# Kernel optimization log

Measured on AMD Instinct MI355X. Metric: run time of the kernel, lower is better.

## Reference

```python
import jax, jax.numpy as jnp
import numpy as np

B, S, D_MODEL = 2, 2048, 2048
NUM_HEADS, KV_HEADS, HEAD_DIM = 16, 4, 128
KV_DIM = KV_HEADS * HEAD_DIM


def apply_rotary_emb(x, cos, sin):
    # x: [B, S, H, D]; cos/sin: [S, 1, D] broadcast over batch and heads
    xr = x.reshape(*x.shape[:-1], HEAD_DIM // 2, 2)
    x_real, x_imag = xr[..., 0], xr[..., 1]
    x_rot = jnp.stack([-x_imag, x_real], axis=-1).reshape(x.shape)
    return x * cos + x_rot * sin


def setup_inputs() -> dict:
    key = jax.random.key(0)
    k0, k1, k2, k3, k4, k5 = jax.random.split(key, 6)
    hidden_states = jax.random.normal(k0, (B, S, D_MODEL), dtype=jnp.float32)
    attention_mask = jnp.ones((B, S), dtype=bool)
    # realistic rotary angles
    inv_freq = 1.0 / (10000.0 ** (jnp.arange(0, HEAD_DIM, 2, dtype=jnp.float32) / HEAD_DIM))
    angles = jnp.arange(S, dtype=jnp.float32)[:, None] * inv_freq[None, :]  # [S, D/2]
    angles = jnp.repeat(angles, 2, axis=-1)[:, None, :]  # [S, 1, D]
    rope_cos = jnp.cos(angles)
    rope_sin = jnp.sin(angles)
    scale = 0.02
    Wq = jax.random.normal(k1, (D_MODEL, D_MODEL), dtype=jnp.float32) * scale
    Wk = jax.random.normal(k2, (D_MODEL, KV_DIM), dtype=jnp.float32) * scale
    Wv = jax.random.normal(k3, (D_MODEL, KV_DIM), dtype=jnp.float32) * scale
    Wo = jax.random.normal(k4, (D_MODEL, D_MODEL), dtype=jnp.float32) * scale
    return {"hidden_states": hidden_states, "attention_mask": attention_mask,
            "rope_cos": rope_cos, "rope_sin": rope_sin,
            "Wq": Wq, "Wk": Wk, "Wv": Wv, "Wo": Wo}


def reference(hidden_states, attention_mask, rope_cos, rope_sin, Wq, Wk, Wv, Wo):
    b, s, _ = hidden_states.shape
    q = (hidden_states @ Wq).reshape(b, s, NUM_HEADS, HEAD_DIM)
    k = (hidden_states @ Wk).reshape(b, s, KV_HEADS, HEAD_DIM)
    v = (hidden_states @ Wv).reshape(b, s, KV_HEADS, HEAD_DIM)
    # self-attention: RoPE on both Q and K (pre-transpose layout [B,S,H,D])
    q = apply_rotary_emb(q, rope_cos, rope_sin)
    k = apply_rotary_emb(k, rope_cos, rope_sin)
    # GQA: repeat KV heads to match query heads
    n_rep = NUM_HEADS // KV_HEADS
    k = jnp.repeat(k, n_rep, axis=2)  # [B, S, H, D]
    v = jnp.repeat(v, n_rep, axis=2)
    scale = HEAD_DIM ** -0.5
    scores = jnp.einsum("bqhd,bkhd->bhqk", q, k) * scale
    mask = attention_mask[:, None, None, :]  # [B,1,1,S] bool, True = attend
    scores = jnp.where(mask, scores, jnp.finfo(scores.dtype).min)
    probs = jax.nn.softmax(scores, axis=-1)
    out = jnp.einsum("bhqk,bkhd->bqhd", probs, v).reshape(b, s, NUM_HEADS * HEAD_DIM)
    return out @ Wo
```

## Files before the change

kernel.cpp:

```cpp
#include <hip/hip_runtime.h>
#include <hip/hip_fp16.h>

#define DM 2048
#define SL 2048
#define NB 2
#define NH 16
#define NKV 4
#define HD 128
#define QKVN 3072
#define ROWS 4096

using f16 = _Float16;
typedef __attribute__((ext_vector_type(8))) f16 f16x8;
typedef __attribute__((ext_vector_type(4))) f16 f16x4;
typedef __attribute__((ext_vector_type(4))) float f32x4;

__device__ __forceinline__ void gload16(const f16* g, f16* l) {
  __builtin_amdgcn_global_load_lds((const __attribute__((address_space(1))) void*)g,
                                   (__attribute__((address_space(3))) void*)l, 16, 0, 0);
}

__global__ __launch_bounds__(256) void cast_f32_f16(const float* __restrict__ src,
                                                    f16* __restrict__ dst, int n4) {
  int i = blockIdx.x * 256 + threadIdx.x;
  if (i < n4) {
    float4 v = reinterpret_cast<const float4*>(src)[i];
    f16x4 o = {(f16)v.x, (f16)v.y, (f16)v.z, (f16)v.w};
    reinterpret_cast<f16x4*>(dst)[i] = o;
  }
}

__global__ __launch_bounds__(256) void transpose_cast(const float* __restrict__ src,
                                                      f16* __restrict__ dst, int N, float sc) {
  __shared__ float tile[32][33];
  int tx = threadIdx.x & 31, ty = threadIdx.x >> 5;
  int n0 = blockIdx.x * 32, k0 = blockIdx.y * 32;
#pragma unroll
  for (int i = 0; i < 32; i += 8)
    tile[ty + i][tx] = src[(size_t)(k0 + ty + i) * N + n0 + tx];
  __syncthreads();
#pragma unroll
  for (int i = 0; i < 32; i += 8)
    dst[(size_t)(n0 + ty + i) * DM + k0 + tx] = (f16)(tile[tx][ty + i] * sc);
}

__global__ __launch_bounds__(256) void transpose_v(const f16* __restrict__ src,
                                                   f16* __restrict__ dst) {
  __shared__ f16 tl[64 * 64];
  char* tlb = (char*)tl;
  int t = threadIdx.x;
  int r0 = blockIdx.y * 64, c0 = blockIdx.x * 64;
  int lr8 = (t & 7) * 8, hr = t >> 3;
#pragma unroll
  for (int i = 0; i < 64; i += 32) {
    f16x8 v = *(const f16x8*)(src + (size_t)(r0 + hr + i) * QKVN + c0 + lr8);
#pragma unroll
    for (int j = 0; j < 8; ++j) {
      int c = lr8 + j, r = hr + i;
      *(f16*)(tlb + ((c * 128 + r * 2) ^ ((c & 7) << 4))) = v[j];
    }
  }
  __syncthreads();
#pragma unroll
  for (int i = 0; i < 64; i += 32) {
    int c = hr + i;
    f16x8 v = *(const f16x8*)(tlb + ((c * 128 + lr8 * 2) ^ ((c & 7) << 4)));
    *(f16x8*)(dst + (size_t)(c0 + c) * ROWS + r0 + lr8) = v;
  }
}

template <typename TO>
__global__ __launch_bounds__(256) void gemm_kernel(const f16* __restrict__ A,
                                                   const f16* __restrict__ Bt,
                                                   TO* __restrict__ C, int K, int ldc) {
  __shared__ f16 la[128 * 32];
  __shared__ f16 lb[128 * 32];
  int nx = gridDim.x;
  int lin = blockIdx.y * nx + blockIdx.x;
  int cpx = (nx * gridDim.y) >> 3;
  int swz = (lin & 7) * cpx + (lin >> 3);
  int bx = swz % nx, by = swz / nx;
  int t = threadIdx.x;
  int w = t >> 6, lane = t & 63, lr = lane & 15, lg = lane >> 4;
  int wr = (w >> 1) * 64, wc = (w & 1) * 64;
  int rowBase = bx * 128, colBase = by * 128;
  const f16* gA = A + (size_t)(rowBase + (t >> 2)) * K + (t & 3) * 8;
  const f16* gB = Bt + (size_t)(colBase + (t >> 2)) * K + (t & 3) * 8;
  f16* laW = la + w * 512;
  f16* lbW = lb + w * 512;
  f32x4 acc[4][4] = {};
  for (int k0 = 0; k0 < K; k0 += 32) {
    __syncthreads();
    gload16(gA, laW);
    gload16(gA + (size_t)64 * K, laW + 2048);
    gload16(gB, lbW);
    gload16(gB + (size_t)64 * K, lbW + 2048);
    gA += 32; gB += 32;
    __syncthreads();
    f16x8 af[4], bf[4];
#pragma unroll
    for (int m = 0; m < 4; ++m) af[m] = *(const f16x8*)&la[(wr + m * 16 + lr) * 32 + lg * 8];
#pragma unroll
    for (int n = 0; n < 4; ++n) bf[n] = *(const f16x8*)&lb[(wc + n * 16 + lr) * 32 + lg * 8];
#pragma unroll
    for (int m = 0; m < 4; ++m)
#pragma unroll
      for (int n = 0; n < 4; ++n)
        acc[m][n] = __builtin_amdgcn_mfma_f32_16x16x32_f16(af[m], bf[n], acc[m][n], 0, 0, 0);
  }
#pragma unroll
  for (int m = 0; m < 4; ++m) {
    int row = rowBase + wr + m * 16 + lg * 4;
#pragma unroll
    for (int n = 0; n < 4; ++n) {
      int col = colBase + wc + n * 16 + lr;
#pragma unroll
      for (int r = 0; r < 4; ++r)
        C[(size_t)(row + r) * ldc + col] = (TO)acc[m][n][r];
    }
  }
}

__global__ __launch_bounds__(256) void rope_kernel(f16* __restrict__ qk,
                                                   const float* __restrict__ ct,
                                                   const float* __restrict__ st) {
  int idx = blockIdx.x * 256 + threadIdx.x;
  int row = idx / 1280;
  int pc = idx - row * 1280;
  int col = pc * 2;
  int d = col & (HD - 1);
  int s = row & (SL - 1);
  float c = ct[s * HD + d], sn = st[s * HD + d];
  f16* p = qk + (size_t)row * QKVN + col;
  float x0 = (float)p[0], x1 = (float)p[1];
  p[0] = (f16)(x0 * c - x1 * sn);
  p[1] = (f16)(x1 * c + x0 * sn);
}

__global__ __launch_bounds__(256) void attn_kernel(const f16* __restrict__ qk,
                                                   const f16* __restrict__ vt,
                                                   f16* __restrict__ out) {
  __shared__ f16 kl[64 * 128];
  __shared__ f16 vl[128 * 64];
  __shared__ f16 pl[4][16 * 64];
  int bh = blockIdx.y;
  int b = bh >> 4, h = bh & 15, kv = h >> 2;
  int qt = blockIdx.x;
  int t = threadIdx.x, w = t >> 6, lane = t & 63, lr = lane & 15, lg = lane >> 4;

  const f16* Qp = qk + (size_t)(b * SL + qt * 64 + w * 16 + lr) * QKVN + h * HD + lg * 8;
  f16x8 qf[4];
#pragma unroll
  for (int kc = 0; kc < 4; ++kc) qf[kc] = *(const f16x8*)(Qp + kc * 32);

  const f16* Kb = qk + (size_t)(b * SL) * QKVN + DM + kv * HD;
  const f16* Vb = vt + (size_t)(kv * HD) * ROWS + b * SL;

  int kr = t >> 4, kc0 = (t & 15) * 8, kswz = (kr & 7) << 4;
  int vr = t >> 3, vc0 = (t & 7) * 8, vswz = (vr & 7) << 4;
  char* klb = (char*)kl;
  char* vlb = (char*)vl;
  char* kwp = klb + kr * 256 + ((kc0 * 2) ^ kswz);
  char* vwp = vlb + vr * 128 + ((vc0 * 2) ^ vswz);

  f16x8 kreg[4], vreg[4];
#define LOADREGS(KT)                                                              \
  do {                                                                            \
    const f16* kbp = Kb + (size_t)((KT) * 64 + kr) * QKVN + kc0;                  \
    const f16* vbp = Vb + (size_t)vr * ROWS + (KT) * 64 + vc0;                    \
    _Pragma("unroll") for (int it = 0; it < 4; ++it)                              \
        kreg[it] = *(const f16x8*)(kbp + (size_t)it * 16 * QKVN);                 \
    _Pragma("unroll") for (int it = 0; it < 4; ++it)                              \
        vreg[it] = *(const f16x8*)(vbp + (size_t)it * 32 * ROWS);                 \
  } while (0)

  float mrun = -1e30f;
  f32x4 oacc[8] = {};
  f32x4 lacc = {};
  const f16x8 ones = {(f16)1, (f16)1, (f16)1, (f16)1, (f16)1, (f16)1, (f16)1, (f16)1};

  char* plb = (char*)pl[w];
  int swzr = (lr & 7) << 4;

  LOADREGS(0);
  for (int kt = 0; kt < SL / 64; ++kt) {
    __syncthreads();
#pragma unroll
    for (int it = 0; it < 4; ++it) *(f16x8*)(kwp + it * 4096) = kreg[it];
#pragma unroll
    for (int it = 0; it < 4; ++it) *(f16x8*)(vwp + it * 4096) = vreg[it];
    __syncthreads();
    if (kt < SL / 64 - 1) LOADREGS(kt + 1);
    f32x4 s[4] = {};
    __builtin_amdgcn_s_setprio(1);
#pragma unroll
    for (int kc = 0; kc < 4; ++kc) {
#pragma unroll
      for (int ct = 0; ct < 4; ++ct) {
        f16x8 kf = *(const f16x8*)(klb + (ct * 16 + lr) * 256 + ((kc * 64 + lg * 16) ^ swzr));
        s[ct] = __builtin_amdgcn_mfma_f32_16x16x32_f16(kf, qf[kc], s[ct], 0, 0, 0);
      }
    }
    __builtin_amdgcn_s_setprio(0);
    float vmax = -1e30f;
#pragma unroll
    for (int ct = 0; ct < 4; ++ct)
      vmax = fmaxf(vmax, fmaxf(fmaxf(s[ct][0], s[ct][1]), fmaxf(s[ct][2], s[ct][3])));
    vmax = fmaxf(vmax, __shfl_xor(vmax, 16, 64));
    vmax = fmaxf(vmax, __shfl_xor(vmax, 32, 64));
    if (!__all(vmax <= mrun + 6.f)) {
      float mnew = fmaxf(mrun, vmax);
      float al = exp2f(mrun - mnew);
#pragma unroll
      for (int dtl = 0; dtl < 8; ++dtl)
#pragma unroll
        for (int r = 0; r < 4; ++r) oacc[dtl][r] *= al;
#pragma unroll
      for (int r = 0; r < 4; ++r) lacc[r] *= al;
      mrun = mnew;
    }
    float m = mrun;
#pragma unroll
    for (int ct = 0; ct < 4; ++ct) {
      f16x4 pv = {(f16)exp2f(s[ct][0] - m), (f16)exp2f(s[ct][1] - m),
                  (f16)exp2f(s[ct][2] - m), (f16)exp2f(s[ct][3] - m)};
      *(f16x4*)(plb + lr * 128 + ((ct * 32 + lg * 8) ^ swzr)) = pv;
    }
    __builtin_amdgcn_s_setprio(1);
#pragma unroll
    for (int kc = 0; kc < 2; ++kc) {
      f16x8 pf = *(const f16x8*)(plb + lr * 128 + ((kc * 64 + lg * 16) ^ swzr));
      lacc = __builtin_amdgcn_mfma_f32_16x16x32_f16(ones, pf, lacc, 0, 0, 0);
#pragma unroll
      for (int dtl = 0; dtl < 8; ++dtl) {
        f16x8 vf = *(const f16x8*)(vlb + (dtl * 16 + lr) * 128 + ((kc * 64 + lg * 16) ^ swzr));
        oacc[dtl] = __builtin_amdgcn_mfma_f32_16x16x32_f16(vf, pf, oacc[dtl], 0, 0, 0);
      }
    }
    __builtin_amdgcn_s_setprio(0);
  }
#undef LOADREGS
  float inv = 1.0f / lacc[0];
  f16* orow = out + (size_t)(b * SL + qt * 64 + w * 16 + lr) * DM + h * HD;
#pragma unroll
  for (int dtl = 0; dtl < 8; ++dtl) {
    f16x4 o = {(f16)(oacc[dtl][0] * inv), (f16)(oacc[dtl][1] * inv),
               (f16)(oacc[dtl][2] * inv), (f16)(oacc[dtl][3] * inv)};
    *(f16x4*)(orow + dtl * 16 + lg * 4) = o;
  }
}

extern "C" void kernel_launch(void* const* d_in, const int* in_sizes, int n_in,
                              void* d_out, int out_size, void* d_ws, size_t ws_size,
                              hipStream_t stream) {
  const float* hidden   = (const float*)d_in[0];
  const float* rope_cos = (const float*)d_in[2];
  const float* rope_sin = (const float*)d_in[3];
  const float* Wq = (const float*)d_in[4];
  const float* Wk = (const float*)d_in[5];
  const float* Wv = (const float*)d_in[6];
  const float* Wo = (const float*)d_in[7];
  float* out = (float*)d_out;

  char* ws = (char*)d_ws;
  f16* hidden_h = (f16*)(ws);
  f16* Wt       = (f16*)(ws + 16777216);
  f16* Wot      = (f16*)(ws + 29360128);
  f16* QKV      = (f16*)(ws + 37748736);
  f16* Vt       = Wt;
  f16* attnO    = hidden_h;

  const float QSC = 0.08838834764831845f * 1.4426950408889634f;

  cast_f32_f16<<<dim3(8192), 256, 0, stream>>>(hidden, hidden_h, 2097152);
  transpose_cast<<<dim3(64, 64), 256, 0, stream>>>(Wq, Wt, 2048, QSC);
  transpose_cast<<<dim3(16, 64), 256, 0, stream>>>(Wk, Wt + (size_t)2048 * 2048, 512, 1.0f);
  transpose_cast<<<dim3(16, 64), 256, 0, stream>>>(Wv, Wt + (size_t)2560 * 2048, 512, 1.0f);
  transpose_cast<<<dim3(64, 64), 256, 0, stream>>>(Wo, Wot, 2048, 1.0f);

  gemm_kernel<f16><<<dim3(32, 24), 256, 0, stream>>>(hidden_h, Wt, QKV, 2048, QKVN);

  transpose_v<<<dim3(8, 64), 256, 0, stream>>>(QKV + 2560, Vt);

  rope_kernel<<<dim3(20480), 256, 0, stream>>>(QKV, rope_cos, rope_sin);

  attn_kernel<<<dim3(32, 32), 256, 0, stream>>>(QKV, Vt, attnO);

  gemm_kernel<float><<<dim3(32, 16), 256, 0, stream>>>(attnO, Wot, out, 2048, 2048);
}
```

Before: 394.7 us.

## Replace 128x128 GEMM with 256x256 tile, 8-wave, double-buffered LDS pipeline

The single-buffered 128x128 GEMM is replaced by a 256x256-tile kernel with 512 threads (8 waves). It double-buffers LDS across k-slices and issues direct global-to-LDS loads for the next stage while MFMAs run, using explicit vmcnt waits, barriers and priority raising. The aim is to hide load latency and raise arithmetic intensity per block in both projection GEMMs. The cost is fewer blocks (192 and 128 on a 256-CU part), so under-occupancy and tail effects are possible, along with high register use from 32 accumulators per wave.

```diff
diff --git a/kernel.cpp b/kernel.cpp
--- a/kernel.cpp
+++ b/kernel.cpp
@@ -70,53 +70,93 @@
 }
 
 template <typename TO>
-__global__ __launch_bounds__(256) void gemm_kernel(const f16* __restrict__ A,
-                                                   const f16* __restrict__ Bt,
-                                                   TO* __restrict__ C, int K, int ldc) {
-  __shared__ f16 la[128 * 32];
-  __shared__ f16 lb[128 * 32];
+__global__ __launch_bounds__(512, 2) void gemm256(const f16* __restrict__ A,
+                                                  const f16* __restrict__ Bt,
+                                                  TO* __restrict__ C, int K, int ldc) {
+  __shared__ __align__(16) f16 lds[2][4][8192];
+  const int t = threadIdx.x;
+  const int w = t >> 6, lane = t & 63;
+  const int wm = w >> 2, wn = w & 3;
+  const int lr = lane & 15, lg = lane >> 4;
   int nx = gridDim.x;
   int lin = blockIdx.y * nx + blockIdx.x;
   int cpx = (nx * gridDim.y) >> 3;
   int swz = (lin & 7) * cpx + (lin >> 3);
   int bx = swz % nx, by = swz / nx;
-  int t = threadIdx.x;
-  int w = t >> 6, lane = t & 63, lr = lane & 15, lg = lane >> 4;
-  int wr = (w >> 1) * 64, wc = (w & 1) * 64;
-  int rowBase = bx * 128, colBase = by * 128;
-  const f16* gA = A + (size_t)(rowBase + (t >> 2)) * K + (t & 3) * 8;
-  const f16* gB = Bt + (size_t)(colBase + (t >> 2)) * K + (t & 3) * 8;
-  f16* laW = la + w * 512;
-  f16* lbW = lb + w * 512;
-  f32x4 acc[4][4] = {};
-  for (int k0 = 0; k0 < K; k0 += 32) {
-    __syncthreads();
-    gload16(gA, laW);
-    gload16(gA + (size_t)64 * K, laW + 2048);
-    gload16(gB, lbW);
-    gload16(gB + (size_t)64 * K, lbW + 2048);
-    gA += 32; gB += 32;
-    __syncthreads();
-    f16x8 af[4], bf[4];
-#pragma unroll
-    for (int m = 0; m < 4; ++m) af[m] = *(const f16x8*)&la[(wr + m * 16 + lr) * 32 + lg * 8];
-#pragma unroll
-    for (int n = 0; n < 4; ++n) bf[n] = *(const f16x8*)&lb[(wc + n * 16 + lr) * 32 + lg * 8];
-#pragma unroll
-    for (int m = 0; m < 4; ++m)
-#pragma unroll
-      for (int n = 0; n < 4; ++n)
-        acc[m][n] = __builtin_amdgcn_mfma_f32_16x16x32_f16(af[m], bf[n], acc[m][n], 0, 0, 0);
-  }
-#pragma unroll
-  for (int m = 0; m < 4; ++m) {
-    int row = rowBase + wr + m * 16 + lg * 4;
+  const int rowBase = bx * 256, colBase = by * 256;
+  const f16* gAs = A + (size_t)(rowBase + w * 16 + lr) * K + lg * 8;
+  const f16* gBs = Bt + (size_t)(colBase + w * 16 + lr) * K + lg * 8;
+
+#define STG(SLOT, UNIT, GSRC, KOFF)                                   \
+  do {                                                                \
+    f16* d_ = &lds[SLOT][UNIT][w * 512];                              \
+    const f16* s_ = (GSRC) + (KOFF);                                  \
+    gload16(s_, d_);                                                  \
+    gload16(s_ + (size_t)128 * K, d_ + 4096);                         \
+  } while (0)
+
+  f32x4 acc[8][4] = {};
+
+#define PHASE(SLOT, KS, MH, STAGE_STMT, VM_STMT)                              \
+  do {                                                                        \
+    const f16* pA_ = &lds[SLOT][KS][(wm * 8 + (MH) * 4) * 512 + lane * 8];    \
+    const f16* pB_ = &lds[SLOT][2 + (KS)][wn * 4 * 512 + lane * 8];           \
+    f16x8 af[4], bf[4];                                                       \
+    _Pragma("unroll") for (int j_ = 0; j_ < 4; ++j_)                          \
+        af[j_] = *(const f16x8*)(pA_ + j_ * 512);                             \
+    _Pragma("unroll") for (int n_ = 0; n_ < 4; ++n_)                          \
+        bf[n_] = *(const f16x8*)(pB_ + n_ * 512);                             \
+    STAGE_STMT;                                                               \
+    VM_STMT;                                                                  \
+    __builtin_amdgcn_s_barrier();                                             \
+    __builtin_amdgcn_sched_barrier(0);                                        \
+    __builtin_amdgcn_s_setprio(1);                                            \
+    _Pragma("unroll") for (int j_ = 0; j_ < 4; ++j_)                          \
+      _Pragma("unroll") for (int n_ = 0; n_ < 4; ++n_)                        \
+        acc[(MH) * 4 + j_][n_] = __builtin_amdgcn_mfma_f32_16x16x32_f16(      \
+            af[j_], bf[n_], acc[(MH) * 4 + j_][n_], 0, 0, 0);                 \
+    __builtin_amdgcn_s_setprio(0);                                            \
+    __builtin_amdgcn_sched_barrier(0);                                        \
+    __builtin_amdgcn_s_barrier();                                             \
+  } while (0)
+
+  const int NIT = K / 128;
+  STG(0, 0, gAs, 0);
+  STG(0, 2, gBs, 0);
+  STG(0, 1, gAs, 32);
+  STG(0, 3, gBs, 32);
+  STG(1, 0, gAs, 64);
+  STG(1, 2, gBs, 64);
+  asm volatile("s_waitcnt vmcnt(4)" ::: "memory");
+  __builtin_amdgcn_s_barrier();
+
+  for (int i = 0; i < NIT; ++i) {
+    const int k0 = i * 128;
+    const bool more = (i + 1 < NIT);
+    PHASE(0, 0, 0, STG(1, 1, gAs, k0 + 96), );
+    PHASE(0, 0, 1, STG(1, 3, gBs, k0 + 96), );
+    PHASE(0, 1, 0, if (more) STG(0, 0, gAs, k0 + 128), );
+    PHASE(0, 1, 1, if (more) STG(0, 2, gBs, k0 + 128),
+          if (more) { asm volatile("s_waitcnt vmcnt(4)" ::: "memory"); }
+          else      { asm volatile("s_waitcnt vmcnt(0)" ::: "memory"); });
+    PHASE(1, 0, 0, if (more) STG(0, 1, gAs, k0 + 160), );
+    PHASE(1, 0, 1, if (more) STG(0, 3, gBs, k0 + 160), );
+    PHASE(1, 1, 0, if (more) STG(1, 0, gAs, k0 + 192), );
+    PHASE(1, 1, 1, if (more) STG(1, 2, gBs, k0 + 192),
+          if (more) { asm volatile("s_waitcnt vmcnt(4)" ::: "memory"); }
+          else      { asm volatile("s_waitcnt vmcnt(0)" ::: "memory"); });
+  }
+#undef PHASE
+#undef STG
+#pragma unroll
+  for (int fr = 0; fr < 8; ++fr) {
+    int row = rowBase + wm * 128 + fr * 16 + lg * 4;
 #pragma unroll
     for (int n = 0; n < 4; ++n) {
-      int col = colBase + wc + n * 16 + lr;
+      int col = colBase + wn * 64 + n * 16 + lr;
 #pragma unroll
       for (int r = 0; r < 4; ++r)
-        C[(size_t)(row + r) * ldc + col] = (TO)acc[m][n][r];
+        C[(size_t)(row + r) * ldc + col] = (TO)acc[fr][n][r];
     }
   }
 }
@@ -278,7 +318,7 @@
   transpose_cast<<<dim3(16, 64), 256, 0, stream>>>(Wv, Wt + (size_t)2560 * 2048, 512, 1.0f);
   transpose_cast<<<dim3(64, 64), 256, 0, stream>>>(Wo, Wot, 2048, 1.0f);
 
-  gemm_kernel<f16><<<dim3(32, 24), 256, 0, stream>>>(hidden_h, Wt, QKV, 2048, QKVN);
+  gemm256<f16><<<dim3(16, 12), 512, 0, stream>>>(hidden_h, Wt, QKV, 2048, QKVN);
 
   transpose_v<<<dim3(8, 64), 256, 0, stream>>>(QKV + 2560, Vt);
 
@@ -286,5 +326,5 @@
 
   attn_kernel<<<dim3(32, 32), 256, 0, stream>>>(QKV, Vt, attnO);
 
-  gemm_kernel<float><<<dim3(32, 16), 256, 0, stream>>>(attnO, Wot, out, 2048, 2048);
-}
+  gemm256<float><<<dim3(16, 8), 512, 0, stream>>>(attnO, Wot, out, 2048, 2048);
+}
```

Measured after the change: 407.5 us. +3.3%, slower.
